# Kernel optimization log

Measured on AMD Instinct MI355X. Metric: run time of the kernel, lower is better.

## Reference

```python
import jax, jax.numpy as jnp
import numpy as np

NEG_INF = jnp.float32(-1e16)


def _gat_layer(x, W, b, graph):
    # x: [B,N,D_in], W: [D_in,D_out], b: [D_out], graph: [N,N]
    h = x @ W  # [B,N,D_out]
    s = jnp.einsum('bnd,bmd->bnm', h, h) * graph  # [B,N,N]
    s = jnp.where(s == 0.0, NEG_INF, s)  # masked_fill(scores==0, -1e16)
    a = jax.nn.softmax(s, axis=-1)
    return jnp.einsum('bnm,bmd->bnd', a, h) + b


def setup_inputs() -> dict:
    key = jax.random.key(0)
    ks = jax.random.split(key, 9)
    B, N, T, C = 2, 2048, 3, 16
    H, HID, OUT = 4, 16, 16
    flow_x = jax.random.normal(ks[0], (B, N, T, C), dtype=jnp.float32)
    graph = jax.random.randint(ks[1], (N, N), 0, 2).astype(jnp.float32)
    W1 = jax.random.normal(ks[2], (T, H, C, HID), dtype=jnp.float32)
    b1 = jax.random.normal(ks[3], (T, H, HID), dtype=jnp.float32)
    W2 = jax.random.normal(ks[4], (T, H * HID, OUT), dtype=jnp.float32)
    b2 = jax.random.normal(ks[5], (T, OUT), dtype=jnp.float32)
    W3 = jax.random.normal(ks[6], (T * OUT, OUT), dtype=jnp.float32)
    b3 = jax.random.normal(ks[7], (OUT,), dtype=jnp.float32)
    return {"flow_x": flow_x, "graph": graph, "W1": W1, "b1": b1,
            "W2": W2, "b2": b2, "W3": W3, "b3": b3}


def reference(flow_x, graph, W1, b1, W2, b2, W3, b3):
    B, N, T, C = flow_x.shape
    leaky = lambda v: jax.nn.leaky_relu(v, negative_slope=0.01)
    outs = []
    for t in range(T):  # static loop over distinct per-timestep subnets
        f = flow_x[:, :, t, :]  # [B,N,C]
        # all heads at once: h: [B,H,N,HID]
        h = jnp.einsum('bnc,hcd->bhnd', f, W1[t])
        s = jnp.einsum('bhnd,bhmd->bhnm', h, h) * graph  # [B,H,N,N]
        s = jnp.where(s == 0.0, NEG_INF, s)
        a = jax.nn.softmax(s, axis=-1)
        r = jnp.einsum('bhnm,bhmd->bhnd', a, h) + b1[t][None, :, None, :]
        # concat heads along feature dim (head-major order like torch.cat)
        r = r.transpose(0, 2, 1, 3).reshape(B, N, -1)  # [B,N,H*HID]
        r = leaky(r)
        r = leaky(_gat_layer(r, W2[t], b2[t], graph))  # [B,N,OUT]
        outs.append(r)
    hidden = jnp.concatenate(outs, axis=2)  # [B,N,T*OUT]
    out = _gat_layer(hidden, W3, b3, graph)  # [B,N,OUT]
    return out[:, :, None, :]  # [B,N,1,OUT]
```

## Files before the change

kernel.cpp:

```cpp
#include <hip/hip_runtime.h>
#include <stdint.h>

static constexpr int N = 2048;
static constexpr int B = 2;
static constexpr int T = 3;
static constexpr int H = 4;
static constexpr int D = 16;
static constexpr float NEG = -1e30f;

__global__ void pack_mask(const float* __restrict__ g, unsigned long long* __restrict__ mb) {
    int idx = blockIdx.x * 256 + threadIdx.x;
    float v = g[idx];
    unsigned long long bal = __ballot(v != 0.0f);
    if ((threadIdx.x & 63) == 0) mb[idx >> 6] = bal;
}

__global__ void k_h1(const float* __restrict__ fx, const float* __restrict__ W1,
                     float* __restrict__ h1) {
    int id = blockIdx.x * 256 + threadIdx.x;
    int n = id & (N - 1);
    int head = id >> 11;
    int t = head >> 3;
    int b = (head >> 2) & 1;
    int h = head & 3;
    const float* f = fx + (((size_t)(b * N + n)) * T + t) * D;
    const float* w = W1 + ((t * H + h) * D) * (size_t)D;
    float fr[D];
    const float4* f4 = (const float4*)f;
#pragma unroll
    for (int k = 0; k < 4; ++k) {
        float4 v = f4[k];
        fr[4*k] = v.x; fr[4*k+1] = v.y; fr[4*k+2] = v.z; fr[4*k+3] = v.w;
    }
    float acc[D] = {};
#pragma unroll
    for (int c = 0; c < D; ++c)
#pragma unroll
        for (int d = 0; d < D; ++d) acc[d] = fmaf(fr[c], w[c*D+d], acc[d]);
    float* o = h1 + (size_t)id * D;
#pragma unroll
    for (int d = 0; d < D; ++d) o[d] = acc[d];
}

template<int KIN, int SHIFT>
__global__ void k_rowmm(const float* __restrict__ x, const float* __restrict__ Wbase,
                        float* __restrict__ y) {
    int id = blockIdx.x * 256 + threadIdx.x;
    const float* __restrict__ xr = x + (size_t)id * KIN;
    const float* __restrict__ w = Wbase + (size_t)(id >> SHIFT) * KIN * D;
    float acc[D] = {};
#pragma unroll
    for (int c4 = 0; c4 < KIN/4; ++c4) {
        float4 xv = ((const float4*)xr)[c4];
        float xs[4] = {xv.x, xv.y, xv.z, xv.w};
#pragma unroll
        for (int q = 0; q < 4; ++q) {
            int c = c4*4 + q;
#pragma unroll
            for (int d = 0; d < D; ++d) acc[d] = fmaf(xs[q], w[c*D+d], acc[d]);
        }
    }
    float* o = y + (size_t)id * D;
#pragma unroll
    for (int d = 0; d < D; ++d) o[d] = acc[d];
}

template<int SPLIT>
__device__ __forceinline__ void attn_slice(
        const float* __restrict__ hh, const uint32_t* __restrict__ mrow,
        const float (&hi)[D], int j0, int jlen,
        float& m, float& l, float (&o)[D]) {
    for (int w = 0; w < jlen/32; ++w) {
        uint32_t mw = mrow[w];
        int jb = j0 + w*32;
#pragma unroll 4
        for (int u = 0; u < 32; ++u) {
            const float4* h4 = (const float4*)(hh + (size_t)(jb + u) * D);
            float4 v0 = h4[0], v1 = h4[1], v2 = h4[2], v3 = h4[3];
            float hj[D];
            hj[0]=v0.x; hj[1]=v0.y; hj[2]=v0.z; hj[3]=v0.w;
            hj[4]=v1.x; hj[5]=v1.y; hj[6]=v1.z; hj[7]=v1.w;
            hj[8]=v2.x; hj[9]=v2.y; hj[10]=v2.z; hj[11]=v2.w;
            hj[12]=v3.x; hj[13]=v3.y; hj[14]=v3.z; hj[15]=v3.w;
            float s0=0.f, s1=0.f, s2=0.f, s3=0.f;
#pragma unroll
            for (int k = 0; k < 4; ++k) {
                s0 = fmaf(hi[k],    hj[k],    s0);
                s1 = fmaf(hi[k+4],  hj[k+4],  s1);
                s2 = fmaf(hi[k+8],  hj[k+8],  s2);
                s3 = fmaf(hi[k+12], hj[k+12], s3);
            }
            float s = (s0 + s1) + (s2 + s3);
            float se = ((mw >> u) & 1u) ? s : NEG;
            if (se > m) {
                float cc = __expf(m - se);
                l *= cc;
#pragma unroll
                for (int k = 0; k < D; ++k) o[k] *= cc;
                m = se;
            }
            float wg = __expf(se - m);
            l += wg;
#pragma unroll
            for (int k = 0; k < D; ++k) o[k] = fmaf(wg, hj[k], o[k]);
        }
    }
}

template<int SPLIT>
__device__ __forceinline__ bool block_merge(
        int lane, int wv, float m, float l, const float (&o)[D],
        float& M, float& L, float (&O)[D]) {
    __shared__ float sm[SPLIT][64];
    __shared__ float sl[SPLIT][64];
    __shared__ float so[SPLIT][64][D+1];
    sm[wv][lane] = m;
    sl[wv][lane] = l;
#pragma unroll
    for (int k = 0; k < D; ++k) so[wv][lane][k] = o[k];
    __syncthreads();
    if (threadIdx.x >= 64) return false;
    int r = threadIdx.x;
    M = sm[0][r];
#pragma unroll
    for (int s = 1; s < SPLIT; ++s) M = fmaxf(M, sm[s][r]);
    L = 0.f;
#pragma unroll
    for (int k = 0; k < D; ++k) O[k] = 0.f;
#pragma unroll
    for (int s = 0; s < SPLIT; ++s) {
        float cc = __expf(sm[s][r] - M);
        L = fmaf(cc, sl[s][r], L);
#pragma unroll
        for (int k = 0; k < D; ++k) O[k] = fmaf(cc, so[s][r][k], O[k]);
    }
    return true;
}

template<int SPLIT>
__global__ __launch_bounds__(64*SPLIT) void attn1(
        const float* __restrict__ hsrc, const uint32_t* __restrict__ mask,
        const float* __restrict__ bias, float* __restrict__ out) {
    constexpr int JLEN = N / SPLIT;
    const int lane = threadIdx.x & 63;
    const int wv = threadIdx.x >> 6;
    const int row = blockIdx.x * 64 + lane;
    const int head = blockIdx.y;
    const float* __restrict__ hh = hsrc + (size_t)head * N * D;

    float hi[D];
    {
        const float4* r4 = (const float4*)(hh + (size_t)row * D);
#pragma unroll
        for (int k = 0; k < 4; ++k) {
            float4 v = r4[k];
            hi[4*k]=v.x; hi[4*k+1]=v.y; hi[4*k+2]=v.z; hi[4*k+3]=v.w;
        }
    }
    const int j0 = __builtin_amdgcn_readfirstlane(wv * JLEN);
    const uint32_t* __restrict__ mrow = mask + (size_t)row * (N/32) + (j0 >> 5);
    float m = NEG, l = 0.f, o[D] = {};
    attn_slice<SPLIT>(hh, mrow, hi, j0, JLEN, m, l, o);

    float M, L, O[D];
    if (block_merge<SPLIT>(lane, wv, m, l, o, M, L, O)) {
        int t = head >> 3, b = (head >> 2) & 1, hd = head & 3;
        const float* bb = bias + (t * H + hd) * D;
        int rr = blockIdx.x * 64 + threadIdx.x;
        float* orow = out + ((size_t)(t * B + b) * N + rr) * (H * D) + hd * D;
        float inv = 1.0f / L;
#pragma unroll
        for (int k = 0; k < D; ++k) {
            float v = fmaf(O[k], inv, bb[k]);
            orow[k] = (v > 0.f) ? v : 0.01f * v;
        }
    }
}

template<int SPLIT, int JS>
__global__ __launch_bounds__(64*SPLIT) void attn_p(
        const float* __restrict__ hsrc, const uint32_t* __restrict__ mask,
        float* __restrict__ pm, float* __restrict__ pl, float* __restrict__ po) {
    constexpr int JLEN = N / (SPLIT * JS);
    static_assert(JLEN >= 32, "mask-word floor");
    const int lane = threadIdx.x & 63;
    const int wv = threadIdx.x >> 6;
    const int row = blockIdx.x * 64 + lane;
    const int head = blockIdx.y;
    const int js = blockIdx.z;
    const float* __restrict__ hh = hsrc + (size_t)head * N * D;

    float hi[D];
    {
        const float4* r4 = (const float4*)(hh + (size_t)row * D);
#pragma unroll
        for (int k = 0; k < 4; ++k) {
            float4 v = r4[k];
            hi[4*k]=v.x; hi[4*k+1]=v.y; hi[4*k+2]=v.z; hi[4*k+3]=v.w;
        }
    }
    const int j0 = __builtin_amdgcn_readfirstlane((js * SPLIT + wv) * JLEN);
    const uint32_t* __restrict__ mrow = mask + (size_t)row * (N/32) + (j0 >> 5);
    float m = NEG, l = 0.f, o[D] = {};
    attn_slice<SPLIT>(hh, mrow, hi, j0, JLEN, m, l, o);

    float M, L, O[D];
    if (block_merge<SPLIT>(lane, wv, m, l, o, M, L, O)) {
        int rr = blockIdx.x * 64 + threadIdx.x;
        size_t pidx = ((size_t)head * N + rr) * JS + js;
        pm[pidx] = M;
        pl[pidx] = L;
#pragma unroll
        for (int k = 0; k < D; ++k) po[pidx * D + k] = O[k];
    }
}

template<int JS, int LAYER, bool LEAKY>
__global__ void k_merge(const float* __restrict__ pm, const float* __restrict__ pl,
                        const float* __restrict__ po, const float* __restrict__ bias,
                        float* __restrict__ out) {
    int id = blockIdx.x * 256 + threadIdx.x;
    int row = id & (N - 1);
    int head = id >> 11;
    size_t base = (size_t)id * JS;
    float M = pm[base];
#pragma unroll
    for (int s = 1; s < JS; ++s) M = fmaxf(M, pm[base + s]);
    float L = 0.f, O[D] = {};
#pragma unroll
    for (int s = 0; s < JS; ++s) {
        float cc = __expf(pm[base + s] - M);
        L = fmaf(cc, pl[base + s], L);
        const float* pp = po + (base + s) * D;
#pragma unroll
        for (int k = 0; k < D; ++k) O[k] = fmaf(cc, pp[k], O[k]);
    }
    const float* bb; float* orow;
    if constexpr (LAYER == 2) {
        int t = head >> 1, b = head & 1;
        bb = bias + t * D;
        orow = out + ((size_t)b * N + row) * (T * D) + t * D;
    } else {
        bb = bias;
        orow = out + ((size_t)head * N + row) * D;
    }
    float inv = 1.0f / L;
#pragma unroll
    for (int k = 0; k < D; ++k) {
        float v = fmaf(O[k], inv, bb[k]);
        if (LEAKY) v = (v > 0.f) ? v : 0.01f * v;
        orow[k] = v;
    }
}

extern "C" void kernel_launch(void* const* d_in, const int* in_sizes, int n_in,
                              void* d_out, int out_size, void* d_ws, size_t ws_size,
                              hipStream_t stream) {
    const float* fx    = (const float*)d_in[0];
    const float* graph = (const float*)d_in[1];
    const float* W1    = (const float*)d_in[2];
    const float* b1    = (const float*)d_in[3];
    const float* W2    = (const float*)d_in[4];
    const float* b2    = (const float*)d_in[5];
    const float* W3    = (const float*)d_in[6];
    const float* b3    = (const float*)d_in[7];
    float* out = (float*)d_out;

    char* ws = (char*)d_ws;
    unsigned long long* mask64 = (unsigned long long*)ws;
    float* h1     = (float*)(ws + (size_t)(N*(size_t)N/8));
    float* x2     = h1 + (size_t)T*B*H*N*D;
    float* h2     = x2 + (size_t)T*B*N*H*D;
    float* hidden = h2 + (size_t)T*B*N*D;
    float* h3     = hidden + (size_t)B*N*T*D;

    constexpr size_t PMAX = (size_t)T*B*N*4;
    float* pm = h1;
    float* pl = h1 + PMAX;
    float* po = h1 + 2*PMAX;

    pack_mask<<<N*N/256, 256, 0, stream>>>(graph, mask64);
    k_h1<<<T*B*H*N/256, 256, 0, stream>>>(fx, W1, h1);

    attn1<8><<<dim3(N/64, T*B*H), 512, 0, stream>>>(h1, (const uint32_t*)mask64, b1, x2);
    k_rowmm<H*D,12><<<T*B*N/256, 256, 0, stream>>>(x2, W2, h2);

    attn_p<8,4><<<dim3(N/64, T*B, 4), 512, 0, stream>>>(h2, (const uint32_t*)mask64, pm, pl, po);
    k_merge<4,2,true><<<T*B*N/256, 256, 0, stream>>>(pm, pl, po, b2, hidden);

    k_rowmm<T*D,20><<<B*N/256, 256, 0, stream>>>(hidden, W3, h3);

    attn_p<8,8><<<dim3(N/64, B, 8), 512, 0, stream>>>(h3, (const uint32_t*)mask64, pm, pl, po);
    k_merge<8,3,false><<<B*N/256, 256, 0, stream>>>(pm, pl, po, b3, out);
}
```

Before: 307.0 us.

## Fuse mask/h1 prep, merge+matmul kernels, lazy rescale with exp2 softmax

Merges mask packing and the first projection into one launch. The layer-1 attention now goes through split-K partials, and each partial-merge kernel also does the next layer's projection, which removes the separate rowmm kernels and the x2/hidden intermediates. The online softmax switches to base-2 exponentials with log2e folded into the query row, and it only rescales when some lane's max grows by more than 64 (a wave-uniform branch), which cuts divergent rescale work. Blocks shrink to 4 waves with more j-splits, chosen by the available workspace size. This adds more partial-state traffic and carries an overflow risk from the lazy-rescale threshold.

```diff
diff --git a/kernel.cpp b/kernel.cpp
--- a/kernel.cpp
+++ b/kernel.cpp
@@ -7,17 +7,19 @@
 static constexpr int H = 4;
 static constexpr int D = 16;
 static constexpr float NEG = -1e30f;
-
-__global__ void pack_mask(const float* __restrict__ g, unsigned long long* __restrict__ mb) {
-    int idx = blockIdx.x * 256 + threadIdx.x;
-    float v = g[idx];
-    unsigned long long bal = __ballot(v != 0.0f);
-    if ((threadIdx.x & 63) == 0) mb[idx >> 6] = bal;
-}
-
-__global__ void k_h1(const float* __restrict__ fx, const float* __restrict__ W1,
-                     float* __restrict__ h1) {
-    int id = blockIdx.x * 256 + threadIdx.x;
+static constexpr float LOG2E = 1.4426950408889634f;
+
+__global__ void k_prep(const float* __restrict__ g, unsigned long long* __restrict__ mb,
+                       const float* __restrict__ fx, const float* __restrict__ W1,
+                       float* __restrict__ h1) {
+    if (blockIdx.x < (unsigned)(N * N / 256)) {
+        int idx = blockIdx.x * 256 + threadIdx.x;
+        float v = g[idx];
+        unsigned long long bal = __ballot(v != 0.0f);
+        if ((threadIdx.x & 63) == 0) mb[idx >> 6] = bal;
+        return;
+    }
+    int id = (blockIdx.x - N * N / 256) * 256 + threadIdx.x;
     int n = id & (N - 1);
     int head = id >> 11;
     int t = head >> 3;
@@ -42,40 +44,16 @@
     for (int d = 0; d < D; ++d) o[d] = acc[d];
 }
 
-template<int KIN, int SHIFT>
-__global__ void k_rowmm(const float* __restrict__ x, const float* __restrict__ Wbase,
-                        float* __restrict__ y) {
-    int id = blockIdx.x * 256 + threadIdx.x;
-    const float* __restrict__ xr = x + (size_t)id * KIN;
-    const float* __restrict__ w = Wbase + (size_t)(id >> SHIFT) * KIN * D;
-    float acc[D] = {};
-#pragma unroll
-    for (int c4 = 0; c4 < KIN/4; ++c4) {
-        float4 xv = ((const float4*)xr)[c4];
-        float xs[4] = {xv.x, xv.y, xv.z, xv.w};
-#pragma unroll
-        for (int q = 0; q < 4; ++q) {
-            int c = c4*4 + q;
-#pragma unroll
-            for (int d = 0; d < D; ++d) acc[d] = fmaf(xs[q], w[c*D+d], acc[d]);
-        }
-    }
-    float* o = y + (size_t)id * D;
-#pragma unroll
-    for (int d = 0; d < D; ++d) o[d] = acc[d];
-}
-
-template<int SPLIT>
 __device__ __forceinline__ void attn_slice(
         const float* __restrict__ hh, const uint32_t* __restrict__ mrow,
         const float (&hi)[D], int j0, int jlen,
         float& m, float& l, float (&o)[D]) {
     for (int w = 0; w < jlen/32; ++w) {
         uint32_t mw = mrow[w];
-        int jb = j0 + w*32;
-#pragma unroll 4
+        const float* __restrict__ tb = hh + (size_t)(j0 + w*32) * D;
+#pragma unroll 8
         for (int u = 0; u < 32; ++u) {
-            const float4* h4 = (const float4*)(hh + (size_t)(jb + u) * D);
+            const float4* h4 = (const float4*)(tb + u*D);
             float4 v0 = h4[0], v1 = h4[1], v2 = h4[2], v3 = h4[3];
             float hj[D];
             hj[0]=v0.x; hj[1]=v0.y; hj[2]=v0.z; hj[3]=v0.w;
@@ -91,19 +69,32 @@
                 s3 = fmaf(hi[k+12], hj[k+12], s3);
             }
             float s = (s0 + s1) + (s2 + s3);
-            float se = ((mw >> u) & 1u) ? s : NEG;
-            if (se > m) {
-                float cc = __expf(m - se);
+            float se = (mw & (1u << u)) ? s : NEG;
+            if (__any(se - m > 64.f)) {
+                float mn = fmaxf(m, se);
+                float cc = __builtin_amdgcn_exp2f(m - mn);
                 l *= cc;
 #pragma unroll
-                for (int k = 0; k < D; ++k) o[k] *= cc;
-                m = se;
+                for (int p = 0; p < D; ++p) o[p] *= cc;
+                m = mn;
             }
-            float wg = __expf(se - m);
+            float wg = __builtin_amdgcn_exp2f(se - m);
             l += wg;
 #pragma unroll
             for (int k = 0; k < D; ++k) o[k] = fmaf(wg, hj[k], o[k]);
         }
+    }
+}
+
+__device__ __forceinline__ void load_hi(const float* __restrict__ hh, int row, float (&hi)[D]) {
+    const float4* r4 = (const float4*)(hh + (size_t)row * D);
+#pragma unroll
+    for (int k = 0; k < 4; ++k) {
+        float4 v = r4[k];
+        hi[4*k]   = v.x * LOG2E;
+        hi[4*k+1] = v.y * LOG2E;
+        hi[4*k+2] = v.z * LOG2E;
+        hi[4*k+3] = v.w * LOG2E;
     }
 }
 
@@ -129,52 +120,12 @@
     for (int k = 0; k < D; ++k) O[k] = 0.f;
 #pragma unroll
     for (int s = 0; s < SPLIT; ++s) {
-        float cc = __expf(sm[s][r] - M);
+        float cc = __builtin_amdgcn_exp2f(sm[s][r] - M);
         L = fmaf(cc, sl[s][r], L);
 #pragma unroll
         for (int k = 0; k < D; ++k) O[k] = fmaf(cc, so[s][r][k], O[k]);
     }
     return true;
-}
-
-template<int SPLIT>
-__global__ __launch_bounds__(64*SPLIT) void attn1(
-        const float* __restrict__ hsrc, const uint32_t* __restrict__ mask,
-        const float* __restrict__ bias, float* __restrict__ out) {
-    constexpr int JLEN = N / SPLIT;
-    const int lane = threadIdx.x & 63;
-    const int wv = threadIdx.x >> 6;
-    const int row = blockIdx.x * 64 + lane;
-    const int head = blockIdx.y;
-    const float* __restrict__ hh = hsrc + (size_t)head * N * D;
-
-    float hi[D];
-    {
-        const float4* r4 = (const float4*)(hh + (size_t)row * D);
-#pragma unroll
-        for (int k = 0; k < 4; ++k) {
-            float4 v = r4[k];
-            hi[4*k]=v.x; hi[4*k+1]=v.y; hi[4*k+2]=v.z; hi[4*k+3]=v.w;
-        }
-    }
-    const int j0 = __builtin_amdgcn_readfirstlane(wv * JLEN);
-    const uint32_t* __restrict__ mrow = mask + (size_t)row * (N/32) + (j0 >> 5);
-    float m = NEG, l = 0.f, o[D] = {};
-    attn_slice<SPLIT>(hh, mrow, hi, j0, JLEN, m, l, o);
-
-    float M, L, O[D];
-    if (block_merge<SPLIT>(lane, wv, m, l, o, M, L, O)) {
-        int t = head >> 3, b = (head >> 2) & 1, hd = head & 3;
-        const float* bb = bias + (t * H + hd) * D;
-        int rr = blockIdx.x * 64 + threadIdx.x;
-        float* orow = out + ((size_t)(t * B + b) * N + rr) * (H * D) + hd * D;
-        float inv = 1.0f / L;
-#pragma unroll
-        for (int k = 0; k < D; ++k) {
-            float v = fmaf(O[k], inv, bb[k]);
-            orow[k] = (v > 0.f) ? v : 0.01f * v;
-        }
-    }
 }
 
 template<int SPLIT, int JS>
@@ -191,18 +142,11 @@
     const float* __restrict__ hh = hsrc + (size_t)head * N * D;
 
     float hi[D];
-    {
-        const float4* r4 = (const float4*)(hh + (size_t)row * D);
-#pragma unroll
-        for (int k = 0; k < 4; ++k) {
-            float4 v = r4[k];
-            hi[4*k]=v.x; hi[4*k+1]=v.y; hi[4*k+2]=v.z; hi[4*k+3]=v.w;
-        }
-    }
+    load_hi(hh, row, hi);
     const int j0 = __builtin_amdgcn_readfirstlane((js * SPLIT + wv) * JLEN);
     const uint32_t* __restrict__ mrow = mask + (size_t)row * (N/32) + (j0 >> 5);
     float m = NEG, l = 0.f, o[D] = {};
-    attn_slice<SPLIT>(hh, mrow, hi, j0, JLEN, m, l, o);
+    attn_slice(hh, mrow, hi, j0, JLEN, m, l, o);
 
     float M, L, O[D];
     if (block_merge<SPLIT>(lane, wv, m, l, o, M, L, O)) {
@@ -215,13 +159,112 @@
     }
 }
 
-template<int JS, int LAYER, bool LEAKY>
-__global__ void k_merge(const float* __restrict__ pm, const float* __restrict__ pl,
-                        const float* __restrict__ po, const float* __restrict__ bias,
-                        float* __restrict__ out) {
+template<int JS>
+__global__ void k_mr1(const float* __restrict__ pm, const float* __restrict__ pl,
+                      const float* __restrict__ po, const float* __restrict__ b1,
+                      const float* __restrict__ W2, float* __restrict__ h2) {
     int id = blockIdx.x * 256 + threadIdx.x;
-    int row = id & (N - 1);
-    int head = id >> 11;
+    int q = id & 3;
+    int tbrow = id >> 2;
+    int row = tbrow & (N - 1);
+    int tb = tbrow >> 11;
+    int t = tb >> 1;
+    float x2[H * D];
+#pragma unroll
+    for (int hd = 0; hd < H; ++hd) {
+        size_t base = ((size_t)(tb * H + hd) * N + row) * JS;
+        float M = pm[base];
+#pragma unroll
+        for (int s = 1; s < JS; ++s) M = fmaxf(M, pm[base + s]);
+        float L = 0.f, O[D] = {};
+#pragma unroll
+        for (int s = 0; s < JS; ++s) {
+            float cc = __builtin_amdgcn_exp2f(pm[base + s] - M);
+            L = fmaf(cc, pl[base + s], L);
+            const float4* pp = (const float4*)(po + (base + s) * D);
+#pragma unroll
+            for (int k4 = 0; k4 < 4; ++k4) {
+                float4 v = pp[k4];
+                O[4*k4]   = fmaf(cc, v.x, O[4*k4]);
+                O[4*k4+1] = fmaf(cc, v.y, O[4*k4+1]);
+                O[4*k4+2] = fmaf(cc, v.z, O[4*k4+2]);
+                O[4*k4+3] = fmaf(cc, v.w, O[4*k4+3]);
+            }
+        }
+        float inv = 1.0f / L;
+        const float* bb = b1 + (t * H + hd) * D;
+#pragma unroll
+        for (int k = 0; k < D; ++k) {
+            float v = fmaf(O[k], inv, bb[k]);
+            x2[hd * D + k] = (v > 0.f) ? v : 0.01f * v;
+        }
+    }
+    const float* w = W2 + (size_t)t * (H * D) * D + q * 4;
+    float acc[4] = {};
+#pragma unroll
+    for (int c = 0; c < H * D; ++c)
+#pragma unroll
+        for (int d = 0; d < 4; ++d) acc[d] = fmaf(x2[c], w[c * D + d], acc[d]);
+    float* outp = h2 + (size_t)tbrow * D + q * 4;
+#pragma unroll
+    for (int d = 0; d < 4; ++d) outp[d] = acc[d];
+}
+
+template<int JS>
+__global__ void k_mr2(const float* __restrict__ pm, const float* __restrict__ pl,
+                      const float* __restrict__ po, const float* __restrict__ b2,
+                      const float* __restrict__ W3, float* __restrict__ h3) {
+    int id = blockIdx.x * 256 + threadIdx.x;
+    int q = id & 3;
+    int brow = id >> 2;
+    int row = brow & (N - 1);
+    int b = brow >> 11;
+    float hid[T * D];
+#pragma unroll
+    for (int t = 0; t < T; ++t) {
+        size_t base = ((size_t)(t * B + b) * N + row) * JS;
+        float M = pm[base];
+#pragma unroll
+        for (int s = 1; s < JS; ++s) M = fmaxf(M, pm[base + s]);
+        float L = 0.f, O[D] = {};
+#pragma unroll
+        for (int s = 0; s < JS; ++s) {
+            float cc = __builtin_amdgcn_exp2f(pm[base + s] - M);
+            L = fmaf(cc, pl[base + s], L);
+            const float4* pp = (const float4*)(po + (base + s) * D);
+#pragma unroll
+            for (int k4 = 0; k4 < 4; ++k4) {
+                float4 v = pp[k4];
+                O[4*k4]   = fmaf(cc, v.x, O[4*k4]);
+                O[4*k4+1] = fmaf(cc, v.y, O[4*k4+1]);
+                O[4*k4+2] = fmaf(cc, v.z, O[4*k4+2]);
+                O[4*k4+3] = fmaf(cc, v.w, O[4*k4+3]);
+            }
+        }
+        float inv = 1.0f / L;
+        const float* bb = b2 + t * D;
+#pragma unroll
+        for (int k = 0; k < D; ++k) {
+            float v = fmaf(O[k], inv, bb[k]);
+            hid[t * D + k] = (v > 0.f) ? v : 0.01f * v;
+        }
+    }
+    const float* w = W3 + q * 4;
+    float acc[4] = {};
+#pragma unroll
+    for (int c = 0; c < T * D; ++c)
+#pragma unroll
+        for (int d = 0; d < 4; ++d) acc[d] = fmaf(hid[c], w[c * D + d], acc[d]);
+    float* outp = h3 + (size_t)brow * D + q * 4;
+#pragma unroll
+    for (int d = 0; d < 4; ++d) outp[d] = acc[d];
+}
+
+template<int JS>
+__global__ void k_merge3(const float* __restrict__ pm, const float* __restrict__ pl,
+                         const float* __restrict__ po, const float* __restrict__ bias,
+                         float* __restrict__ out) {
+    int id = blockIdx.x * 256 + threadIdx.x;
     size_t base = (size_t)id * JS;
     float M = pm[base];
 #pragma unroll
@@ -229,28 +272,33 @@
     float L = 0.f, O[D] = {};
 #pragma unroll
     for (int s = 0; s < JS; ++s) {
-        float cc = __expf(pm[base + s] - M);
+        float cc = __builtin_amdgcn_exp2f(pm[base + s] - M);
         L = fmaf(cc, pl[base + s], L);
         const float* pp = po + (base + s) * D;
 #pragma unroll
         for (int k = 0; k < D; ++k) O[k] = fmaf(cc, pp[k], O[k]);
     }
-    const float* bb; float* orow;
-    if constexpr (LAYER == 2) {
-        int t = head >> 1, b = head & 1;
-        bb = bias + t * D;
-        orow = out + ((size_t)b * N + row) * (T * D) + t * D;
-    } else {
-        bb = bias;
-        orow = out + ((size_t)head * N + row) * D;
-    }
     float inv = 1.0f / L;
-#pragma unroll
-    for (int k = 0; k < D; ++k) {
-        float v = fmaf(O[k], inv, bb[k]);
-        if (LEAKY) v = (v > 0.f) ? v : 0.01f * v;
-        orow[k] = v;
-    }
+    float* orow = out + (size_t)id * D;
+#pragma unroll
+    for (int k = 0; k < D; ++k) orow[k] = fmaf(O[k], inv, bias[k]);
+}
+
+template<int JS1>
+static void run_pipeline(const float* graph, const float* fx,
+                         const float* W1, const float* b1, const float* W2,
+                         const float* b2, const float* W3, const float* b3,
+                         float* out, unsigned long long* mask64, float* h1,
+                         float* h2, float* h3, float* pm, float* pl, float* po,
+                         hipStream_t stream) {
+    const uint32_t* mk = (const uint32_t*)mask64;
+    k_prep<<<N*N/256 + T*B*H*N/256, 256, 0, stream>>>(graph, mask64, fx, W1, h1);
+    attn_p<4,JS1><<<dim3(N/64, T*B*H, JS1), 256, 0, stream>>>(h1, mk, pm, pl, po);
+    k_mr1<JS1><<<T*B*N*4/256, 256, 0, stream>>>(pm, pl, po, b1, W2, h2);
+    attn_p<4,8><<<dim3(N/64, T*B, 8), 256, 0, stream>>>(h2, mk, pm, pl, po);
+    k_mr2<8><<<B*N*4/256, 256, 0, stream>>>(pm, pl, po, b2, W3, h3);
+    attn_p<4,16><<<dim3(N/64, B, 16), 256, 0, stream>>>(h3, mk, pm, pl, po);
+    k_merge3<16><<<B*N/256, 256, 0, stream>>>(pm, pl, po, b3, out);
 }
 
 extern "C" void kernel_launch(void* const* d_in, const int* in_sizes, int n_in,
@@ -268,28 +316,28 @@
 
     char* ws = (char*)d_ws;
     unsigned long long* mask64 = (unsigned long long*)ws;
-    float* h1     = (float*)(ws + (size_t)(N*(size_t)N/8));
-    float* x2     = h1 + (size_t)T*B*H*N*D;
-    float* h2     = x2 + (size_t)T*B*N*H*D;
-    float* hidden = h2 + (size_t)T*B*N*D;
-    float* h3     = hidden + (size_t)B*N*T*D;
-
-    constexpr size_t PMAX = (size_t)T*B*N*4;
-    float* pm = h1;
-    float* pl = h1 + PMAX;
-    float* po = h1 + 2*PMAX;
-
-    pack_mask<<<N*N/256, 256, 0, stream>>>(graph, mask64);
-    k_h1<<<T*B*H*N/256, 256, 0, stream>>>(fx, W1, h1);
-
-    attn1<8><<<dim3(N/64, T*B*H), 512, 0, stream>>>(h1, (const uint32_t*)mask64, b1, x2);
-    k_rowmm<H*D,12><<<T*B*N/256, 256, 0, stream>>>(x2, W2, h2);
-
-    attn_p<8,4><<<dim3(N/64, T*B, 4), 512, 0, stream>>>(h2, (const uint32_t*)mask64, pm, pl, po);
-    k_merge<4,2,true><<<T*B*N/256, 256, 0, stream>>>(pm, pl, po, b2, hidden);
-
-    k_rowmm<T*D,20><<<B*N/256, 256, 0, stream>>>(hidden, W3, h3);
-
-    attn_p<8,8><<<dim3(N/64, B, 8), 512, 0, stream>>>(h3, (const uint32_t*)mask64, pm, pl, po);
-    k_merge<8,3,false><<<B*N/256, 256, 0, stream>>>(pm, pl, po, b3, out);
-}
+    float* h1 = (float*)(ws + (size_t)(N*(size_t)N/8));
+    float* h2 = h1 + (size_t)T*B*H*N*D;
+    float* h3 = h2 + (size_t)T*B*N*D;
+    float* tail = h3 + (size_t)B*N*D;
+
+    constexpr size_t P8 = (size_t)T*B*H*N*8;
+    constexpr size_t P4 = (size_t)T*B*H*N*4;
+    constexpr size_t P2 = (size_t)T*B*H*N*2;
+    size_t need8 = (char*)(tail + P8*(2 + D)) - ws;
+    size_t need4 = (char*)(tail + P4*(2 + D)) - ws;
+
+    if (ws_size >= need8) {
+        float *pm = tail, *pl = tail + P8, *po = tail + 2*P8;
+        run_pipeline<8>(graph, fx, W1, b1, W2, b2, W3, b3, out,
+                        mask64, h1, h2, h3, pm, pl, po, stream);
+    } else if (ws_size >= need4) {
+        float *pm = tail, *pl = tail + P4, *po = tail + 2*P4;
+        run_pipeline<4>(graph, fx, W1, b1, W2, b2, W3, b3, out,
+                        mask64, h1, h2, h3, pm, pl, po, stream);
+    } else {
+        float *pm = tail, *pl = tail + P2, *po = tail + 2*P2;
+        run_pipeline<2>(graph, fx, W1, b1, W2, b2, W3, b3, out,
+                        mask64, h1, h2, h3, pm, pl, po, stream);
+    }
+}
```

Measured after the change: 297.9 us. -3.0%, faster.
